# Performance work log

Measured on AMD Instinct MI355X. Metric: run time of the kernel, lower is better.

The kernel has to match this reference:

```python
import jax, jax.numpy as jnp
import numpy as np

BATCH, N_CONCEPTS, EMBED_DIM = 16384, 4096, 64
CURVATURE = 1.0
EPS = 1e-7
BALL_SCALE = 0.05  # keep points inside the Poincare ball (c*||x||^2 < 1)


def setup_inputs() -> dict:
    key = jax.random.key(0)
    k1, k2 = jax.random.split(key)
    embeddings = BALL_SCALE * jax.random.normal(k1, (BATCH, EMBED_DIM), dtype=jnp.float32)
    prototypes = BALL_SCALE * jax.random.normal(k2, (N_CONCEPTS, EMBED_DIM), dtype=jnp.float32)
    return {"embeddings": embeddings, "prototypes": prototypes}


def poincare_pairwise(x, p, c):
    # x: (B, D) points, p: (N, D) prototypes -> (B, N) hyperbolic distances.
    # d(x,y) = (1/sqrt(c)) * acosh(1 + 2c*||x-y||^2 / ((1 - c||x||^2)(1 - c||y||^2)))
    x2 = jnp.sum(x * x, axis=-1)                     # (B,)
    p2 = jnp.sum(p * p, axis=-1)                     # (N,)
    xp = x @ p.T                                     # (B, N) single fused GEMM
    sq = jnp.maximum(x2[:, None] + p2[None, :] - 2.0 * xp, 0.0)  # (B, N)
    denom = jnp.maximum((1.0 - c * x2)[:, None] * (1.0 - c * p2)[None, :], EPS)
    arg = 1.0 + 2.0 * c * sq / denom
    return jnp.arccosh(jnp.maximum(arg, 1.0 + EPS)) / jnp.sqrt(c)


def reference(embeddings, prototypes) -> jnp.ndarray:
    # Vectorized equivalent of the per-concept Python loop over prototypes.
    return poincare_pairwise(embeddings, prototypes, CURVATURE)  # (B, N)
```

## Files before the change

### kernel.cpp

```cpp
#include <hip/hip_runtime.h>
#include <hip/hip_bf16.h>


constexpr int BATCH = 16384;
constexpr int NCON  = 4096;
constexpr int DIM   = 64;
constexpr int TM    = 64;
constexpr int TN    = 128;
constexpr int NT_N  = NCON / TN;
constexpr float LN2 = 0.6931471805599453f;

typedef float  f32x4  __attribute__((ext_vector_type(4)));
typedef __bf16 bf16x8 __attribute__((ext_vector_type(8)));

__global__ __launch_bounds__(256, 4)
void poincare_pairwise_kernel(const float* __restrict__ emb,
                              const float* __restrict__ proto,
                              float* __restrict__ out)
{
    __shared__ __bf16 As[TM * DIM];
    __shared__ __bf16 Bs[TN * DIM];
    __shared__ float  x2s[TM];
    __shared__ float  p2s[TN];
    __shared__ float  rps[TN];

    const int tid = threadIdx.x;
    const int bid = blockIdx.x;
    const int mt  = bid >> 5;
    const int nt  = bid & (NT_N - 1);
    const int m0  = mt * TM;
    const int n0  = nt * TN;

    #pragma unroll
    for (int p = 0; p < 4; ++p) {
        int flat = p * 256 + tid;
        int row  = flat >> 4;
        int kq   = flat & 15;
        f32x4 v = *reinterpret_cast<const f32x4*>(emb + (size_t)(m0 + row) * DIM + kq * 4);
        float ss = v.x * v.x + v.y * v.y + v.z * v.z + v.w * v.w;
        ss += __shfl_xor(ss, 1);
        ss += __shfl_xor(ss, 2);
        ss += __shfl_xor(ss, 4);
        ss += __shfl_xor(ss, 8);
        if (kq == 0) x2s[row] = ss;
        __bf16 b4[4] = {(__bf16)v.x, (__bf16)v.y, (__bf16)v.z, (__bf16)v.w};
        int ke = (kq * 4) ^ ((row & 7) << 3);
        *reinterpret_cast<uint2*>(&As[row * DIM + ke]) = *reinterpret_cast<const uint2*>(b4);
    }
    #pragma unroll
    for (int p = 0; p < 8; ++p) {
        int flat = p * 256 + tid;
        int row  = flat >> 4;
        int kq   = flat & 15;
        f32x4 v = *reinterpret_cast<const f32x4*>(proto + (size_t)(n0 + row) * DIM + kq * 4);
        float ss = v.x * v.x + v.y * v.y + v.z * v.z + v.w * v.w;
        ss += __shfl_xor(ss, 1);
        ss += __shfl_xor(ss, 2);
        ss += __shfl_xor(ss, 4);
        ss += __shfl_xor(ss, 8);
        if (kq == 0) {
            p2s[row] = ss;
            rps[row] = __builtin_amdgcn_rcpf(1.0f - ss);
        }
        __bf16 b4[4] = {(__bf16)v.x, (__bf16)v.y, (__bf16)v.z, (__bf16)v.w};
        int ke = (kq * 4) ^ ((row & 7) << 3);
        *reinterpret_cast<uint2*>(&Bs[row * DIM + ke]) = *reinterpret_cast<const uint2*>(b4);
    }
    __syncthreads();

    const int lane = tid & 63;
    const int wid  = tid >> 6;
    const int lr   = lane & 15;
    const int g    = lane >> 4;
    const int lk   = g * 8;

    bf16x8 xfrag[2];
    #pragma unroll
    for (int kk = 0; kk < 2; ++kk) {
        int xrow = wid * 16 + lr;
        int ke   = (kk * 32 + lk) ^ ((xrow & 7) << 3);
        xfrag[kk] = *reinterpret_cast<const bf16x8*>(&As[xrow * DIM + ke]);
    }

    f32x4 acc[8] = {};
    #pragma unroll
    for (int kk = 0; kk < 2; ++kk) {
        bf16x8 pfrag[8];
        #pragma unroll
        for (int pf = 0; pf < 8; ++pf) {
            int prow = pf * 16 + lr;
            int kep  = (kk * 32 + lk) ^ ((prow & 7) << 3);
            pfrag[pf] = *reinterpret_cast<const bf16x8*>(&Bs[prow * DIM + kep]);
        }
        #pragma unroll
        for (int pf = 0; pf < 8; ++pf)
            acc[pf] = __builtin_amdgcn_mfma_f32_16x16x32_bf16(
                pfrag[pf], xfrag[kk], acc[pf], 0, 0, 0);
    }

    const float x2   = x2s[wid * 16 + lr];
    const float crow = 2.0f * __builtin_amdgcn_rcpf(1.0f - x2);
    float* rowp = out + (size_t)(m0 + wid * 16 + lr) * NCON + n0;
    #pragma unroll
    for (int pf = 0; pf < 8; ++pf) {
        int   col = pf * 16 + g * 4;
        f32x4 p2  = *reinterpret_cast<const f32x4*>(&p2s[col]);
        f32x4 rp  = *reinterpret_cast<const f32x4*>(&rps[col]);
        f32x4 dv;
        #pragma unroll
        for (int j = 0; j < 4; ++j) {
            float xp = acc[pf][j];
            float sq = fmaxf(x2 + p2[j] - 2.0f * xp, 0.0f);
            float t  = sq * crow * rp[j];
            float s  = __builtin_amdgcn_sqrtf(t * (t + 2.0f));
            dv[j]    = LN2 * __builtin_amdgcn_logf(1.0f + t + s);
        }
        *reinterpret_cast<f32x4*>(rowp + col) = dv;
    }
}

extern "C" void kernel_launch(void* const* d_in, const int* in_sizes, int n_in,
                              void* d_out, int out_size, void* d_ws, size_t ws_size,
                              hipStream_t stream) {
    const float* emb   = (const float*)d_in[0];
    const float* proto = (const float*)d_in[1];
    float* out = (float*)d_out;

    dim3 grid((BATCH / TM) * (NCON / TN));
    dim3 block(256);
    poincare_pairwise_kernel<<<grid, block, 0, stream>>>(emb, proto, out);
}
```

Baseline: 72.82 us.

## Make blocks persistent over a prototype band with double-buffered tile prefetch

Each block now keeps a 128-row embedding tile resident and loops over 8 prototype tiles of 64 columns. It prefetches the next prototype tile into registers and stages it into a second shared buffer while the current tile is computed and written. This cuts the per-block setup cost, the embedding reloads and the block count (8192 down to 1024), and aims to overlap global loads with MFMA and epilogue work. The risks are fewer blocks, which lowers latency hiding, plus extra register pressure under launch_bounds(256,4). The kernel is dominated by its 256MB output write, so the upside is limited.

```diff
diff --git a/kernel.cpp b/kernel.cpp
--- a/kernel.cpp
+++ b/kernel.cpp
@@ -5,9 +5,10 @@
 constexpr int BATCH = 16384;
 constexpr int NCON  = 4096;
 constexpr int DIM   = 64;
-constexpr int TM    = 64;
-constexpr int TN    = 128;
-constexpr int NT_N  = NCON / TN;
+constexpr int TM    = 128;
+constexpr int TN    = 64;
+constexpr int NTILE = 8;
+constexpr int BAND  = TN * NTILE;
 constexpr float LN2 = 0.6931471805599453f;
 
 typedef float  f32x4  __attribute__((ext_vector_type(4)));
@@ -19,25 +20,28 @@
                               float* __restrict__ out)
 {
     __shared__ __bf16 As[TM * DIM];
-    __shared__ __bf16 Bs[TN * DIM];
+    __shared__ __bf16 Bs[2][TN * DIM];
     __shared__ float  x2s[TM];
-    __shared__ float  p2s[TN];
-    __shared__ float  rps[TN];
+    __shared__ float  p2s[2][TN];
+    __shared__ float  rps[2][TN];
 
-    const int tid = threadIdx.x;
-    const int bid = blockIdx.x;
-    const int mt  = bid >> 5;
-    const int nt  = bid & (NT_N - 1);
-    const int m0  = mt * TM;
-    const int n0  = nt * TN;
+    const int tid  = threadIdx.x;
+    const int bid  = blockIdx.x;
+    const int m0   = (bid >> 3) * TM;
+    const int n0   = (bid & 7) * BAND;
+
+    const int lane = tid & 63;
+    const int wid  = tid >> 6;
+    const int lr   = lane & 15;
+    const int g    = lane >> 4;
+    const int lk   = g * 8;
 
     #pragma unroll
-    for (int p = 0; p < 4; ++p) {
+    for (int p = 0; p < 8; ++p) {
         int flat = p * 256 + tid;
-        int row  = flat >> 4;
-        int kq   = flat & 15;
+        int row  = flat >> 4, kq = flat & 15;
         f32x4 v = *reinterpret_cast<const f32x4*>(emb + (size_t)(m0 + row) * DIM + kq * 4);
-        float ss = v.x * v.x + v.y * v.y + v.z * v.z + v.w * v.w;
+        float ss = v.x*v.x + v.y*v.y + v.z*v.z + v.w*v.w;
         ss += __shfl_xor(ss, 1);
         ss += __shfl_xor(ss, 2);
         ss += __shfl_xor(ss, 4);
@@ -48,74 +52,108 @@
         *reinterpret_cast<uint2*>(&As[row * DIM + ke]) = *reinterpret_cast<const uint2*>(b4);
     }
     #pragma unroll
-    for (int p = 0; p < 8; ++p) {
+    for (int p = 0; p < 4; ++p) {
         int flat = p * 256 + tid;
-        int row  = flat >> 4;
-        int kq   = flat & 15;
+        int row  = flat >> 4, kq = flat & 15;
         f32x4 v = *reinterpret_cast<const f32x4*>(proto + (size_t)(n0 + row) * DIM + kq * 4);
-        float ss = v.x * v.x + v.y * v.y + v.z * v.z + v.w * v.w;
+        float ss = v.x*v.x + v.y*v.y + v.z*v.z + v.w*v.w;
         ss += __shfl_xor(ss, 1);
         ss += __shfl_xor(ss, 2);
         ss += __shfl_xor(ss, 4);
         ss += __shfl_xor(ss, 8);
-        if (kq == 0) {
-            p2s[row] = ss;
-            rps[row] = __builtin_amdgcn_rcpf(1.0f - ss);
-        }
+        if (kq == 0) { p2s[0][row] = ss; rps[0][row] = __builtin_amdgcn_rcpf(1.0f - ss); }
         __bf16 b4[4] = {(__bf16)v.x, (__bf16)v.y, (__bf16)v.z, (__bf16)v.w};
         int ke = (kq * 4) ^ ((row & 7) << 3);
-        *reinterpret_cast<uint2*>(&Bs[row * DIM + ke]) = *reinterpret_cast<const uint2*>(b4);
+        *reinterpret_cast<uint2*>(&Bs[0][row * DIM + ke]) = *reinterpret_cast<const uint2*>(b4);
     }
     __syncthreads();
 
-    const int lane = tid & 63;
-    const int wid  = tid >> 6;
-    const int lr   = lane & 15;
-    const int g    = lane >> 4;
-    const int lk   = g * 8;
-
-    bf16x8 xfrag[2];
+    bf16x8 xfrag[2][2];
+    float  x2[2], crow[2];
+    float* rowp[2];
     #pragma unroll
-    for (int kk = 0; kk < 2; ++kk) {
-        int xrow = wid * 16 + lr;
-        int ke   = (kk * 32 + lk) ^ ((xrow & 7) << 3);
-        xfrag[kk] = *reinterpret_cast<const bf16x8*>(&As[xrow * DIM + ke]);
+    for (int rf = 0; rf < 2; ++rf) {
+        int xrow = rf * 64 + wid * 16 + lr;
+        #pragma unroll
+        for (int kk = 0; kk < 2; ++kk) {
+            int ke = (kk * 32 + lk) ^ ((xrow & 7) << 3);
+            xfrag[kk][rf] = *reinterpret_cast<const bf16x8*>(&As[xrow * DIM + ke]);
+        }
+        x2[rf]   = x2s[xrow];
+        crow[rf] = 2.0f * __builtin_amdgcn_rcpf(1.0f - x2[rf]);
+        rowp[rf] = out + (size_t)(m0 + xrow) * NCON + n0;
     }
 
-    f32x4 acc[8] = {};
-    #pragma unroll
-    for (int kk = 0; kk < 2; ++kk) {
-        bf16x8 pfrag[8];
+    int cur = 0;
+    #pragma unroll 2
+    for (int t = 0; t < NTILE; ++t) {
+        f32x4 pv[4];
+        if (t < NTILE - 1) {
+            const float* pbase = proto + (size_t)(n0 + (t + 1) * TN) * DIM;
+            #pragma unroll
+            for (int p = 0; p < 4; ++p) {
+                int flat = p * 256 + tid;
+                pv[p] = *reinterpret_cast<const f32x4*>(pbase + (flat >> 4) * DIM + (flat & 15) * 4);
+            }
+        }
+
+        f32x4 acc[2][4] = {};
         #pragma unroll
-        for (int pf = 0; pf < 8; ++pf) {
-            int prow = pf * 16 + lr;
-            int kep  = (kk * 32 + lk) ^ ((prow & 7) << 3);
-            pfrag[pf] = *reinterpret_cast<const bf16x8*>(&Bs[prow * DIM + kep]);
+        for (int kk = 0; kk < 2; ++kk) {
+            bf16x8 pfrag[4];
+            #pragma unroll
+            for (int pf = 0; pf < 4; ++pf) {
+                int prow = pf * 16 + lr;
+                int kep  = (kk * 32 + lk) ^ ((prow & 7) << 3);
+                pfrag[pf] = *reinterpret_cast<const bf16x8*>(&Bs[cur][prow * DIM + kep]);
+            }
+            #pragma unroll
+            for (int pf = 0; pf < 4; ++pf) {
+                acc[0][pf] = __builtin_amdgcn_mfma_f32_16x16x32_bf16(pfrag[pf], xfrag[kk][0], acc[0][pf], 0, 0, 0);
+                acc[1][pf] = __builtin_amdgcn_mfma_f32_16x16x32_bf16(pfrag[pf], xfrag[kk][1], acc[1][pf], 0, 0, 0);
+            }
         }
+
         #pragma unroll
-        for (int pf = 0; pf < 8; ++pf)
-            acc[pf] = __builtin_amdgcn_mfma_f32_16x16x32_bf16(
-                pfrag[pf], xfrag[kk], acc[pf], 0, 0, 0);
-    }
+        for (int pf = 0; pf < 4; ++pf) {
+            int   col = pf * 16 + g * 4;
+            f32x4 p2  = *reinterpret_cast<const f32x4*>(&p2s[cur][col]);
+            f32x4 rp  = *reinterpret_cast<const f32x4*>(&rps[cur][col]);
+            #pragma unroll
+            for (int rf = 0; rf < 2; ++rf) {
+                f32x4 dv;
+                #pragma unroll
+                for (int j = 0; j < 4; ++j) {
+                    float xpp = x2[rf] + p2[j];
+                    float crp = crow[rf] * rp[j];
+                    float sq  = fmaxf(xpp - 2.0f * acc[rf][pf][j], 0.0f);
+                    float tt  = sq * crp;
+                    float s   = __builtin_amdgcn_sqrtf(tt * (tt + 2.0f));
+                    dv[j]     = LN2 * __builtin_amdgcn_logf(1.0f + tt + s);
+                }
+                *reinterpret_cast<f32x4*>(rowp[rf] + t * TN + col) = dv;
+            }
+        }
 
-    const float x2   = x2s[wid * 16 + lr];
-    const float crow = 2.0f * __builtin_amdgcn_rcpf(1.0f - x2);
-    float* rowp = out + (size_t)(m0 + wid * 16 + lr) * NCON + n0;
-    #pragma unroll
-    for (int pf = 0; pf < 8; ++pf) {
-        int   col = pf * 16 + g * 4;
-        f32x4 p2  = *reinterpret_cast<const f32x4*>(&p2s[col]);
-        f32x4 rp  = *reinterpret_cast<const f32x4*>(&rps[col]);
-        f32x4 dv;
-        #pragma unroll
-        for (int j = 0; j < 4; ++j) {
-            float xp = acc[pf][j];
-            float sq = fmaxf(x2 + p2[j] - 2.0f * xp, 0.0f);
-            float t  = sq * crow * rp[j];
-            float s  = __builtin_amdgcn_sqrtf(t * (t + 2.0f));
-            dv[j]    = LN2 * __builtin_amdgcn_logf(1.0f + t + s);
+        if (t < NTILE - 1) {
+            #pragma unroll
+            for (int p = 0; p < 4; ++p) {
+                int flat = p * 256 + tid;
+                int row  = flat >> 4, kq = flat & 15;
+                f32x4 v  = pv[p];
+                float ss = v.x*v.x + v.y*v.y + v.z*v.z + v.w*v.w;
+                ss += __shfl_xor(ss, 1);
+                ss += __shfl_xor(ss, 2);
+                ss += __shfl_xor(ss, 4);
+                ss += __shfl_xor(ss, 8);
+                if (kq == 0) { p2s[cur ^ 1][row] = ss; rps[cur ^ 1][row] = __builtin_amdgcn_rcpf(1.0f - ss); }
+                __bf16 b4[4] = {(__bf16)v.x, (__bf16)v.y, (__bf16)v.z, (__bf16)v.w};
+                int ke = (kq * 4) ^ ((row & 7) << 3);
+                *reinterpret_cast<uint2*>(&Bs[cur ^ 1][row * DIM + ke]) = *reinterpret_cast<const uint2*>(b4);
+            }
+            __syncthreads();
+            cur ^= 1;
         }
-        *reinterpret_cast<f32x4*>(rowp + col) = dv;
     }
 }
 
@@ -126,7 +164,7 @@
     const float* proto = (const float*)d_in[1];
     float* out = (float*)d_out;
 
-    dim3 grid((BATCH / TM) * (NCON / TN));
+    dim3 grid((BATCH / TM) * (NCON / BAND));
     dim3 block(256);
     poincare_pairwise_kernel<<<grid, block, 0, stream>>>(emb, proto, out);
 }
```

After: 96.49 us. 1.33x slower.

## Precompute bf16 swizzled tiles and row norms in a prepass kernel

Applied to the files above, without the earlier changes.

Adds a prepass kernel that converts embeddings and prototypes to bf16 once, in the pre-swizzled tile layout, and computes the squared norms and reciprocal factors into workspace. The main kernel then copies the tiles straight into LDS and reads the per-row and per-column scalars from global memory. This removes the repeated fp32 loads, conversions and shuffle reductions done by every block, since each prototype tile was reloaded by 256 blocks. It costs an extra kernel launch plus a workspace round trip. The epilogue now reads p2 and rp from global memory (likely cache-resident) instead of LDS.

```diff
diff --git a/kernel.cpp b/kernel.cpp
--- a/kernel.cpp
+++ b/kernel.cpp
@@ -7,81 +7,120 @@
 constexpr int DIM   = 64;
 constexpr int TM    = 64;
 constexpr int TN    = 128;
-constexpr int NT_N  = NCON / TN;
 constexpr float LN2 = 0.6931471805599453f;
+
+constexpr size_t WS_EMB   = 0;
+constexpr size_t WS_PROTO = (size_t)2 << 20;
+constexpr size_t WS_X2    = WS_PROTO + (512u << 10);
+constexpr size_t WS_CROW  = WS_X2   + 64u * 1024;
+constexpr size_t WS_P2    = WS_CROW + 64u * 1024;
+constexpr size_t WS_RP    = WS_P2   + 16u * 1024;
 
 typedef float  f32x4  __attribute__((ext_vector_type(4)));
 typedef __bf16 bf16x8 __attribute__((ext_vector_type(8)));
 
+__global__ __launch_bounds__(256)
+void prepass_kernel(const float* __restrict__ emb,
+                    const float* __restrict__ proto,
+                    char* __restrict__ ws)
+{
+    int gid = blockIdx.x * 256 + threadIdx.x;
+    if (gid < 131072) {
+        int c = gid;
+        int mt = c >> 9, within = c & 511;
+        int e0  = within * 8;
+        int row = e0 >> 6;
+        int k0  = (e0 & 63) ^ ((row & 7) << 3);
+        const float* src = emb + (size_t)(mt * 64 + row) * DIM + k0;
+        f32x4 a = *reinterpret_cast<const f32x4*>(src);
+        f32x4 b = *reinterpret_cast<const f32x4*>(src + 4);
+        bf16x8 v;
+        v[0]=(__bf16)a.x; v[1]=(__bf16)a.y; v[2]=(__bf16)a.z; v[3]=(__bf16)a.w;
+        v[4]=(__bf16)b.x; v[5]=(__bf16)b.y; v[6]=(__bf16)b.z; v[7]=(__bf16)b.w;
+        *reinterpret_cast<bf16x8*>(ws + WS_EMB + (size_t)c * 16) = v;
+    } else if (gid < 163840) {
+        int c = gid - 131072;
+        int nt = c >> 10, within = c & 1023;
+        int e0  = within * 8;
+        int row = e0 >> 6;
+        int k0  = (e0 & 63) ^ ((row & 7) << 3);
+        const float* src = proto + (size_t)(nt * 128 + row) * DIM + k0;
+        f32x4 a = *reinterpret_cast<const f32x4*>(src);
+        f32x4 b = *reinterpret_cast<const f32x4*>(src + 4);
+        bf16x8 v;
+        v[0]=(__bf16)a.x; v[1]=(__bf16)a.y; v[2]=(__bf16)a.z; v[3]=(__bf16)a.w;
+        v[4]=(__bf16)b.x; v[5]=(__bf16)b.y; v[6]=(__bf16)b.z; v[7]=(__bf16)b.w;
+        *reinterpret_cast<bf16x8*>(ws + WS_PROTO + (size_t)c * 16) = v;
+    } else if (gid < 180224) {
+        int r = gid - 163840;
+        const f32x4* src = reinterpret_cast<const f32x4*>(emb + (size_t)r * DIM);
+        float s = 0.0f;
+        #pragma unroll
+        for (int i = 0; i < 16; ++i) {
+            f32x4 v = src[i];
+            s += v.x*v.x + v.y*v.y + v.z*v.z + v.w*v.w;
+        }
+        reinterpret_cast<float*>(ws + WS_X2)[r]   = s;
+        reinterpret_cast<float*>(ws + WS_CROW)[r] = 2.0f * __builtin_amdgcn_rcpf(1.0f - s);
+    } else if (gid < 184320) {
+        int r = gid - 180224;
+        const f32x4* src = reinterpret_cast<const f32x4*>(proto + (size_t)r * DIM);
+        float s = 0.0f;
+        #pragma unroll
+        for (int i = 0; i < 16; ++i) {
+            f32x4 v = src[i];
+            s += v.x*v.x + v.y*v.y + v.z*v.z + v.w*v.w;
+        }
+        reinterpret_cast<float*>(ws + WS_P2)[r] = s;
+        reinterpret_cast<float*>(ws + WS_RP)[r] = __builtin_amdgcn_rcpf(1.0f - s);
+    }
+}
+
 __global__ __launch_bounds__(256, 4)
-void poincare_pairwise_kernel(const float* __restrict__ emb,
-                              const float* __restrict__ proto,
+void poincare_pairwise_kernel(const char* __restrict__ ws,
                               float* __restrict__ out)
 {
     __shared__ __bf16 As[TM * DIM];
     __shared__ __bf16 Bs[TN * DIM];
-    __shared__ float  x2s[TM];
-    __shared__ float  p2s[TN];
-    __shared__ float  rps[TN];
 
     const int tid = threadIdx.x;
     const int bid = blockIdx.x;
     const int mt  = bid >> 5;
-    const int nt  = bid & (NT_N - 1);
+    const int nt  = bid & 31;
     const int m0  = mt * TM;
     const int n0  = nt * TN;
 
-    #pragma unroll
-    for (int p = 0; p < 4; ++p) {
-        int flat = p * 256 + tid;
-        int row  = flat >> 4;
-        int kq   = flat & 15;
-        f32x4 v = *reinterpret_cast<const f32x4*>(emb + (size_t)(m0 + row) * DIM + kq * 4);
-        float ss = v.x * v.x + v.y * v.y + v.z * v.z + v.w * v.w;
-        ss += __shfl_xor(ss, 1);
-        ss += __shfl_xor(ss, 2);
-        ss += __shfl_xor(ss, 4);
-        ss += __shfl_xor(ss, 8);
-        if (kq == 0) x2s[row] = ss;
-        __bf16 b4[4] = {(__bf16)v.x, (__bf16)v.y, (__bf16)v.z, (__bf16)v.w};
-        int ke = (kq * 4) ^ ((row & 7) << 3);
-        *reinterpret_cast<uint2*>(&As[row * DIM + ke]) = *reinterpret_cast<const uint2*>(b4);
+    {
+        const uint4* esrc = reinterpret_cast<const uint4*>(ws + WS_EMB + (size_t)mt * 8192);
+        uint4* edst = reinterpret_cast<uint4*>(As);
+        edst[tid]       = esrc[tid];
+        edst[256 + tid] = esrc[256 + tid];
+        const uint4* psrc = reinterpret_cast<const uint4*>(ws + WS_PROTO + (size_t)nt * 16384);
+        uint4* pdst = reinterpret_cast<uint4*>(Bs);
+        #pragma unroll
+        for (int i = 0; i < 4; ++i)
+            pdst[i * 256 + tid] = psrc[i * 256 + tid];
     }
-    #pragma unroll
-    for (int p = 0; p < 8; ++p) {
-        int flat = p * 256 + tid;
-        int row  = flat >> 4;
-        int kq   = flat & 15;
-        f32x4 v = *reinterpret_cast<const f32x4*>(proto + (size_t)(n0 + row) * DIM + kq * 4);
-        float ss = v.x * v.x + v.y * v.y + v.z * v.z + v.w * v.w;
-        ss += __shfl_xor(ss, 1);
-        ss += __shfl_xor(ss, 2);
-        ss += __shfl_xor(ss, 4);
-        ss += __shfl_xor(ss, 8);
-        if (kq == 0) {
-            p2s[row] = ss;
-            rps[row] = __builtin_amdgcn_rcpf(1.0f - ss);
-        }
-        __bf16 b4[4] = {(__bf16)v.x, (__bf16)v.y, (__bf16)v.z, (__bf16)v.w};
-        int ke = (kq * 4) ^ ((row & 7) << 3);
-        *reinterpret_cast<uint2*>(&Bs[row * DIM + ke]) = *reinterpret_cast<const uint2*>(b4);
-    }
-    __syncthreads();
 
     const int lane = tid & 63;
     const int wid  = tid >> 6;
     const int lr   = lane & 15;
     const int g    = lane >> 4;
     const int lk   = g * 8;
+    const int xrow = wid * 16 + lr;
+
+    const float x2   = reinterpret_cast<const float*>(ws + WS_X2)[m0 + xrow];
+    const float crow = reinterpret_cast<const float*>(ws + WS_CROW)[m0 + xrow];
+    float* rowp = out + (size_t)(m0 + xrow) * NCON + n0;
+
+    __syncthreads();
 
     bf16x8 xfrag[2];
     #pragma unroll
     for (int kk = 0; kk < 2; ++kk) {
-        int xrow = wid * 16 + lr;
-        int ke   = (kk * 32 + lk) ^ ((xrow & 7) << 3);
+        int ke = (kk * 32 + lk) ^ ((xrow & 7) << 3);
         xfrag[kk] = *reinterpret_cast<const bf16x8*>(&As[xrow * DIM + ke]);
     }
-
     f32x4 acc[8] = {};
     #pragma unroll
     for (int kk = 0; kk < 2; ++kk) {
@@ -98,22 +137,20 @@
                 pfrag[pf], xfrag[kk], acc[pf], 0, 0, 0);
     }
 
-    const float x2   = x2s[wid * 16 + lr];
-    const float crow = 2.0f * __builtin_amdgcn_rcpf(1.0f - x2);
-    float* rowp = out + (size_t)(m0 + wid * 16 + lr) * NCON + n0;
+    const float* p2a = reinterpret_cast<const float*>(ws + WS_P2) + n0;
+    const float* rpa = reinterpret_cast<const float*>(ws + WS_RP) + n0;
     #pragma unroll
     for (int pf = 0; pf < 8; ++pf) {
         int   col = pf * 16 + g * 4;
-        f32x4 p2  = *reinterpret_cast<const f32x4*>(&p2s[col]);
-        f32x4 rp  = *reinterpret_cast<const f32x4*>(&rps[col]);
+        f32x4 p2  = *reinterpret_cast<const f32x4*>(p2a + col);
+        f32x4 rp  = *reinterpret_cast<const f32x4*>(rpa + col);
         f32x4 dv;
         #pragma unroll
         for (int j = 0; j < 4; ++j) {
-            float xp = acc[pf][j];
-            float sq = fmaxf(x2 + p2[j] - 2.0f * xp, 0.0f);
-            float t  = sq * crow * rp[j];
-            float s  = __builtin_amdgcn_sqrtf(t * (t + 2.0f));
-            dv[j]    = LN2 * __builtin_amdgcn_logf(1.0f + t + s);
+            float sq = fmaxf(x2 + p2[j] - 2.0f * acc[pf][j], 0.0f);
+            float tt = sq * (crow * rp[j]);
+            float s  = __builtin_amdgcn_sqrtf(tt * (tt + 2.0f));
+            dv[j]    = LN2 * __builtin_amdgcn_logf(1.0f + tt + s);
         }
         *reinterpret_cast<f32x4*>(rowp + col) = dv;
     }
@@ -125,8 +162,9 @@
     const float* emb   = (const float*)d_in[0];
     const float* proto = (const float*)d_in[1];
     float* out = (float*)d_out;
+    char* ws   = (char*)d_ws;
 
+    prepass_kernel<<<720, 256, 0, stream>>>(emb, proto, ws);
     dim3 grid((BATCH / TM) * (NCON / TN));
-    dim3 block(256);
-    poincare_pairwise_kernel<<<grid, block, 0, stream>>>(emb, proto, out);
+    poincare_pairwise_kernel<<<grid, 256, 0, stream>>>(ws, out);
 }
```

Result: faster. 65.50 us (-10.0%).
